# Performance work log

Measured on AMD Instinct MI355X. Metric: run time of the kernel, lower is better.

## Reference

```python
import jax, jax.numpy as jnp
import numpy as np

# Config (matches init_kwargs)
COV_DIM = 4
EMBED = 64
E = 256            # key_value_size / MHA embed dim
LH = 512           # lstm_hidden_dim
NH = 8             # num_heads
DH = E // NH
PS = 48            # predict_steps
START = 336        # predict_start
IN1 = 1 + COV_DIM + EMBED + E  # lstm1 input size = 325


def lstm_cell(x, h, c, w_ih, w_hh, b_ih, b_hh):
    gates = x @ w_ih.T + b_ih + h @ w_hh.T + b_hh
    i, f, g, o = jnp.split(gates, 4, axis=-1)
    c = jax.nn.sigmoid(f) * c + jax.nn.sigmoid(i) * jnp.tanh(g)
    h = jax.nn.sigmoid(o) * jnp.tanh(c)
    return h, c


def setup_inputs() -> dict:
    key = jax.random.key(0)
    ks = jax.random.split(key, 24)
    B, T = 512, 336
    s = 0.05
    return {
        "zxs": jax.random.normal(ks[0], (B, START + PS, 1 + COV_DIM), jnp.float32),
        "key": jax.random.normal(ks[1], (B, T, E), jnp.float32),
        "value": jax.random.normal(ks[2], (B, T, E), jnp.float32),
        "idx_embed": jax.random.normal(ks[3], (B, EMBED), jnp.float32),
        # lstm1: input IN1 -> hidden LH
        "w_ih1": jax.random.normal(ks[4], (4 * LH, IN1), jnp.float32) * s,
        "w_hh1": jax.random.normal(ks[5], (4 * LH, LH), jnp.float32) * s,
        "b_ih1": jax.random.normal(ks[6], (4 * LH,), jnp.float32) * s,
        "b_hh1": jax.random.normal(ks[7], (4 * LH,), jnp.float32) * s,
        # lstm2: input LH -> hidden E
        "w_ih2": jax.random.normal(ks[8], (4 * E, LH), jnp.float32) * s,
        "w_hh2": jax.random.normal(ks[9], (4 * E, E), jnp.float32) * s,
        "b_ih2": jax.random.normal(ks[10], (4 * E,), jnp.float32) * s,
        "b_hh2": jax.random.normal(ks[11], (4 * E,), jnp.float32) * s,
        # MultiheadAttention packed in-proj (q,k,v) + out proj
        "in_proj_w": jax.random.normal(ks[12], (3 * E, E), jnp.float32) * s,
        "in_proj_b": jax.random.normal(ks[13], (3 * E,), jnp.float32) * s,
        "out_proj_w": jax.random.normal(ks[14], (E, E), jnp.float32) * s,
        "out_proj_b": jax.random.normal(ks[15], (E,), jnp.float32) * s,
        # heads: Linear(2E -> 1)
        "mu_w": jax.random.normal(ks[16], (1, 2 * E), jnp.float32) * s,
        "mu_b": jax.random.normal(ks[17], (1,), jnp.float32) * s,
        "ps_w": jax.random.normal(ks[18], (1, 2 * E), jnp.float32) * s,
        "ps_b": jax.random.normal(ks[19], (1,), jnp.float32) * s,
    }


def reference(zxs, key, value, idx_embed,
              w_ih1, w_hh1, b_ih1, b_hh1,
              w_ih2, w_hh2, b_ih2, b_hh2,
              in_proj_w, in_proj_b, out_proj_w, out_proj_b,
              mu_w, mu_b, ps_w, ps_b):
    B, T, _ = key.shape
    dt = key.dtype
    wq, wk, wv = jnp.split(in_proj_w, 3, axis=0)
    bq, bk, bv = jnp.split(in_proj_b, 3)
    # K/V projections are constant across decode steps: hoist out of loop.
    kp = (key @ wk.T + bk).reshape(B, T, NH, DH).transpose(0, 2, 1, 3)   # (B,H,T,DH)
    vp = (value @ wv.T + bv).reshape(B, T, NH, DH).transpose(0, 2, 1, 3)  # (B,H,T,DH)
    xs = zxs[:, START:START + PS, :].transpose(1, 0, 2)  # (PS,B,1+cov)
    scale = 1.0 / np.sqrt(DH).astype(np.float32)

    carry0 = (jnp.zeros((B, LH), dt), jnp.zeros((B, LH), dt),
              jnp.zeros((B, E), dt), jnp.zeros((B, E), dt),
              jnp.zeros((B, E), dt))

    def step(carry, x):
        h1, c1, h2, c2, ctx = carry
        inp = jnp.concatenate([x, idx_embed, ctx], axis=1)
        h1, c1 = lstm_cell(inp, h1, c1, w_ih1, w_hh1, b_ih1, b_hh1)
        h2, c2 = lstm_cell(h1, h2, c2, w_ih2, w_hh2, b_ih2, b_hh2)
        # single-query multihead cross-attention (dropout=eval/identity)
        q = (h2 @ wq.T + bq).reshape(B, NH, DH)
        attn = jax.nn.softmax(jnp.einsum('bhd,bhtd->bht', q, kp) * scale, axis=-1)
        ctx = jnp.einsum('bht,bhtd->bhd', attn, vp).reshape(B, E) @ out_proj_w.T + out_proj_b
        oc = jnp.concatenate([h2, ctx], axis=1)  # (B, 2E)
        mu = oc @ mu_w.T + mu_b                  # (B,1)
        sigma = jax.nn.softplus(oc @ ps_w.T + ps_b)
        attn_avg = attn.mean(axis=1)             # head-averaged weights (B,T)
        return (h1, c1, h2, c2, ctx), (mu[:, 0], sigma[:, 0], attn_avg[0])

    _, (mus, sigmas, attns) = jax.lax.scan(step, carry0, xs)
    pred_mu = mus.T        # (B, PS)
    pred_sigma = sigmas.T  # (B, PS)
    attentions = attns.T   # (T, PS) -- matches torch.stack(list of (T,), dim=1)
    return pred_mu, pred_sigma, attentions
```

## Files before the change

### kernel.cpp

```cpp
#include <hip/hip_runtime.h>
#include <hip/hip_bf16.h>

#define BB    512
#define TTT   336
#define EE    256
#define LHH   512
#define NHH   8
#define DHH   32
#define PSS   48
#define STARTT 336
#define NCOV  5
#define XW1   352
#define KP1   864
#define KP2   768
#define COFF  69

typedef __hip_bfloat16 bf16;
typedef __bf16 bf16x8 __attribute__((ext_vector_type(8)));
typedef float  f32x4  __attribute__((ext_vector_type(4)));

__device__ __forceinline__ float sigf(float x) { return 1.f / (1.f + __expf(-x)); }
__device__ __forceinline__ float bf2lo(unsigned u) { return __uint_as_float(u << 16); }
__device__ __forceinline__ float bf2hi(unsigned u) { return __uint_as_float(u & 0xffff0000u); }

__global__ void k_zero(float* __restrict__ p, int n) {
    for (int i = blockIdx.x * blockDim.x + threadIdx.x; i < n; i += gridDim.x * blockDim.x)
        p[i] = 0.f;
}

__global__ void k_cvt_wc1(const float* __restrict__ wih, const float* __restrict__ whh,
                          bf16* __restrict__ Wc) {
    int i = blockIdx.x * blockDim.x + threadIdx.x;
    if (i >= 2048 * KP1) return;
    int n = i / KP1, k = i % KP1;
    float v = (k < 325) ? wih[n * 325 + k] : ((k >= 352) ? whh[n * 512 + (k - 352)] : 0.f);
    Wc[i] = __float2bfloat16(v);
}

__global__ void k_cvt_wc2(const float* __restrict__ wih, const float* __restrict__ whh,
                          bf16* __restrict__ Wc) {
    int i = blockIdx.x * blockDim.x + threadIdx.x;
    if (i >= 1024 * KP2) return;
    int n = i / KP2, k = i % KP2;
    float v = (k < 512) ? wih[n * 512 + k] : whh[n * 256 + (k - 512)];
    Wc[i] = __float2bfloat16(v);
}

__global__ void k_cvt(const float* __restrict__ src, bf16* __restrict__ dst, int n) {
    int i = blockIdx.x * blockDim.x + threadIdx.x;
    if (i < n) dst[i] = __float2bfloat16(src[i]);
}

__global__ void k_bsum(const float* __restrict__ a, const float* __restrict__ b,
                       float* __restrict__ o, int n) {
    int i = blockIdx.x * blockDim.x + threadIdx.x;
    if (i < n) o[i] = a[i] + b[i];
}

__global__ void k_init_xh1(bf16* __restrict__ xh1, const float* __restrict__ idx_embed,
                           const float* __restrict__ zxs) {
    int i = blockIdx.x * blockDim.x + threadIdx.x;
    if (i >= BB * XW1) return;
    int b = i / XW1, k = i % XW1;
    float v = 0.f;
    if (k < NCOV)      v = zxs[b * ((STARTT + PSS) * NCOV) + STARTT * NCOV + k];
    else if (k < COFF) v = idx_embed[b * 64 + (k - NCOV)];
    xh1[i] = __float2bfloat16(v);
}

template<int H, int K0T, int K1T>
__global__ __launch_bounds__(256)
void k_lstm_step(const bf16* __restrict__ A0, int ld0,
                 const bf16* __restrict__ A1, int ld1,
                 const bf16* __restrict__ Wc, const float* __restrict__ bsum,
                 float* __restrict__ c, bf16* __restrict__ hdst,
                 float* __restrict__ outF) {
    constexpr int KP = (K0T + K1T) * 32;
    __shared__ __align__(16) bf16 As[64 * 32];
    __shared__ __align__(16) bf16 Bs[256 * 32];
    const int tid = threadIdx.x;
    const int w = tid >> 6, l = tid & 63;
    const int row0 = blockIdx.x * 64, col0 = blockIdx.y * 64;
    const int srow = tid >> 2, schunk = tid & 3;
    const int fr = l & 15, fc = l >> 4;
    f32x4 acc[16] = {};

    for (int kt = 0; kt < K0T + K1T; ++kt) {
        {
            const bf16* base = (kt < K0T) ? A0 : A1;
            const int ldx    = (kt < K0T) ? ld0 : ld1;
            const int kk     = (kt < K0T) ? kt : (kt - K0T);
            uint4 va = *(const uint4*)(base + (size_t)(row0 + srow) * ldx + kk * 32 + schunk * 8);
            *(uint4*)(As + srow * 32 + (((schunk + (srow >> 1)) & 3) << 3)) = va;
        }
        #pragma unroll
        for (int i = 0; i < 4; ++i) {
            int n = i * 64 + srow;
            int gr = (n >> 6) * H + col0 + (n & 63);
            uint4 vb = *(const uint4*)(Wc + (size_t)gr * KP + kt * 32 + schunk * 8);
            *(uint4*)(Bs + n * 32 + (((schunk + (n >> 1)) & 3) << 3)) = vb;
        }
        __syncthreads();
        const int ar = w * 16 + fr;
        bf16x8 a = *(const bf16x8*)(As + ar * 32 + (((fc + (ar >> 1)) & 3) << 3));
        #pragma unroll
        for (int nt = 0; nt < 16; ++nt) {
            const int br = nt * 16 + fr;
            bf16x8 b = *(const bf16x8*)(Bs + br * 32 + (((fc + (br >> 1)) & 3) << 3));
            acc[nt] = __builtin_amdgcn_mfma_f32_16x16x32_bf16(a, b, acc[nt], 0, 0, 0);
        }
        __syncthreads();
    }

    #pragma unroll
    for (int u = 0; u < 4; ++u) {
        const int hu = col0 + u * 16 + fr;
        const float bi = bsum[hu], bff = bsum[H + hu], bg = bsum[2 * H + hu], bo = bsum[3 * H + hu];
        #pragma unroll
        for (int r = 0; r < 4; ++r) {
            const int R = row0 + w * 16 + fc * 4 + r;
            float gi = acc[u][r]      + bi;
            float gf = acc[4 + u][r]  + bff;
            float gg = acc[8 + u][r]  + bg;
            float go = acc[12 + u][r] + bo;
            float cn = sigf(gf) * c[(size_t)R * H + hu] + sigf(gi) * tanhf(gg);
            c[(size_t)R * H + hu] = cn;
            float h = sigf(go) * tanhf(cn);
            hdst[(size_t)R * H + hu] = __float2bfloat16(h);
            if (outF) outF[(size_t)R * H + hu] = h;
        }
    }
}

__global__ __launch_bounds__(256)
void k_kvproj(const float* __restrict__ X, const bf16* __restrict__ Wb,
              const float* __restrict__ bias, bf16* __restrict__ out) {
    __shared__ __align__(16) bf16 As[64 * 32];
    __shared__ __align__(16) bf16 Bs[256 * 32];
    const int tid = threadIdx.x;
    const int w = tid >> 6, l = tid & 63;
    const int row0 = blockIdx.x * 64;
    const int srow = tid >> 2, schunk = tid & 3;
    const int fr = l & 15, fc = l >> 4;
    f32x4 acc[16] = {};

    for (int kt = 0; kt < 8; ++kt) {
        {
            const float* ap = X + (size_t)(row0 + srow) * EE + kt * 32 + schunk * 8;
            float4 v0 = *(const float4*)ap, v1 = *(const float4*)(ap + 4);
            union { bf16 h[8]; uint4 u; } pk;
            pk.h[0] = __float2bfloat16(v0.x); pk.h[1] = __float2bfloat16(v0.y);
            pk.h[2] = __float2bfloat16(v0.z); pk.h[3] = __float2bfloat16(v0.w);
            pk.h[4] = __float2bfloat16(v1.x); pk.h[5] = __float2bfloat16(v1.y);
            pk.h[6] = __float2bfloat16(v1.z); pk.h[7] = __float2bfloat16(v1.w);
            *(uint4*)(As + srow * 32 + (((schunk + (srow >> 1)) & 3) << 3)) = pk.u;
        }
        #pragma unroll
        for (int i = 0; i < 4; ++i) {
            int n = i * 64 + srow;
            uint4 vb = *(const uint4*)(Wb + (size_t)n * EE + kt * 32 + schunk * 8);
            *(uint4*)(Bs + n * 32 + (((schunk + (n >> 1)) & 3) << 3)) = vb;
        }
        __syncthreads();
        const int ar = w * 16 + fr;
        bf16x8 a = *(const bf16x8*)(As + ar * 32 + (((fc + (ar >> 1)) & 3) << 3));
        #pragma unroll
        for (int nt = 0; nt < 16; ++nt) {
            const int br = nt * 16 + fr;
            bf16x8 b = *(const bf16x8*)(Bs + br * 32 + (((fc + (br >> 1)) & 3) << 3));
            acc[nt] = __builtin_amdgcn_mfma_f32_16x16x32_bf16(a, b, acc[nt], 0, 0, 0);
        }
        __syncthreads();
    }
    #pragma unroll
    for (int nt = 0; nt < 16; ++nt) {
        const int col = nt * 16 + fr;
        const float bv = bias[col];
        #pragma unroll
        for (int r = 0; r < 4; ++r) {
            const int R = row0 + w * 16 + fc * 4 + r;
            out[(size_t)R * EE + col] = __float2bfloat16(acc[nt][r] + bv);
        }
    }
}

__global__ __launch_bounds__(256)
void k_attn_out(const float* __restrict__ h2f, const float* __restrict__ wq, const float* __restrict__ bq,
                const bf16* __restrict__ kp, const bf16* __restrict__ vp,
                const float* __restrict__ opw, const float* __restrict__ opb,
                const float* __restrict__ mu_w, const float* __restrict__ mu_b,
                const float* __restrict__ ps_w, const float* __restrict__ ps_b,
                const float* __restrict__ zxs, bf16* __restrict__ xh1,
                float* __restrict__ out_mu, float* __restrict__ out_sigma,
                float* __restrict__ attn_out, int step) {
    const int b = blockIdx.x;
    const int tid = threadIdx.x;
    __shared__ float h2s[EE];
    __shared__ float qs[EE];
    __shared__ float s[NHH][TTT];
    __shared__ float rm[4], rp[4];

    h2s[tid] = h2f[(size_t)b * EE + tid];
    __syncthreads();

    {
        const float* wr = wq + (size_t)tid * EE;
        float acc = bq[tid];
        #pragma unroll 8
        for (int i = 0; i < EE; ++i) acc += h2s[i] * wr[i];
        qs[tid] = acc * 0.17677669529663689f;
    }
    __syncthreads();

    for (int p = tid; p < NHH * TTT; p += 256) {
        const int h = p / TTT, t = p % TTT;
        const uint4* kr = reinterpret_cast<const uint4*>(kp + ((size_t)(b * TTT + t)) * EE + h * DHH);
        const float* qh = qs + h * DHH;
        float acc = 0.f;
        #pragma unroll
        for (int r = 0; r < 4; ++r) {
            uint4 v = kr[r];
            acc += bf2lo(v.x) * qh[8 * r + 0] + bf2hi(v.x) * qh[8 * r + 1];
            acc += bf2lo(v.y) * qh[8 * r + 2] + bf2hi(v.y) * qh[8 * r + 3];
            acc += bf2lo(v.z) * qh[8 * r + 4] + bf2hi(v.z) * qh[8 * r + 5];
            acc += bf2lo(v.w) * qh[8 * r + 6] + bf2hi(v.w) * qh[8 * r + 7];
        }
        s[h][t] = acc;
    }
    __syncthreads();

    {
        const int wv = tid >> 6, lane = tid & 63;
        for (int hh = 0; hh < 2; ++hh) {
            const int h = wv * 2 + hh;
            float m = -1e30f;
            for (int t = lane; t < TTT; t += 64) m = fmaxf(m, s[h][t]);
            #pragma unroll
            for (int o = 32; o; o >>= 1) m = fmaxf(m, __shfl_xor(m, o));
            float sum = 0.f;
            for (int t = lane; t < TTT; t += 64) {
                float e = __expf(s[h][t] - m);
                s[h][t] = e;
                sum += e;
            }
            #pragma unroll
            for (int o = 32; o; o >>= 1) sum += __shfl_xor(sum, o);
            const float inv = 1.f / sum;
            for (int t = lane; t < TTT; t += 64) s[h][t] *= inv;
        }
    }
    __syncthreads();

    if (b == 0) {
        for (int t = tid; t < TTT; t += 256) {
            float a = 0.f;
            #pragma unroll
            for (int h = 0; h < NHH; ++h) a += s[h][t];
            attn_out[t * PSS + step] = a * 0.125f;
        }
    }

    float av;
    {
        const int h = tid >> 5, d = tid & 31;
        const bf16* vb = vp + (size_t)b * TTT * EE + h * DHH + d;
        float acc = 0.f;
        #pragma unroll 8
        for (int t = 0; t < TTT; ++t)
            acc += s[h][t] * __bfloat162float(vb[(size_t)t * EE]);
        av = acc;
    }
    qs[tid] = av;
    __syncthreads();

    {
        const float* wr = opw + (size_t)tid * EE;
        float ctxv = opb[tid];
        #pragma unroll 8
        for (int i = 0; i < EE; ++i) ctxv += qs[i] * wr[i];
        xh1[(size_t)b * XW1 + COFF + tid] = __float2bfloat16(ctxv);

        const float hv = h2s[tid];
        float pm = hv * mu_w[tid] + ctxv * mu_w[EE + tid];
        float pp = hv * ps_w[tid] + ctxv * ps_w[EE + tid];
        #pragma unroll
        for (int o = 32; o; o >>= 1) {
            pm += __shfl_xor(pm, o);
            pp += __shfl_xor(pp, o);
        }
        const int wv = tid >> 6, lane = tid & 63;
        if (lane == 0) { rm[wv] = pm; rp[wv] = pp; }
    }
    __syncthreads();
    if (tid == 0) {
        float m = rm[0] + rm[1] + rm[2] + rm[3] + mu_b[0];
        float p = rp[0] + rp[1] + rp[2] + rp[3] + ps_b[0];
        out_mu[b * PSS + step] = m;
        out_sigma[b * PSS + step] = (p > 20.f) ? p : log1pf(__expf(p));
    }

    if (tid < NCOV && step + 1 < PSS)
        xh1[(size_t)b * XW1 + tid] =
            __float2bfloat16(zxs[b * ((STARTT + PSS) * NCOV) + (STARTT + step + 1) * NCOV + tid]);
}

extern "C" void kernel_launch(void* const* d_in, const int* in_sizes, int n_in,
                              void* d_out, int out_size, void* d_ws, size_t ws_size,
                              hipStream_t stream) {
    const float* zxs       = (const float*)d_in[0];
    const float* key       = (const float*)d_in[1];
    const float* value     = (const float*)d_in[2];
    const float* idx_embed = (const float*)d_in[3];
    const float* w_ih1     = (const float*)d_in[4];
    const float* w_hh1     = (const float*)d_in[5];
    const float* b_ih1     = (const float*)d_in[6];
    const float* b_hh1     = (const float*)d_in[7];
    const float* w_ih2     = (const float*)d_in[8];
    const float* w_hh2     = (const float*)d_in[9];
    const float* b_ih2     = (const float*)d_in[10];
    const float* b_hh2     = (const float*)d_in[11];
    const float* in_proj_w = (const float*)d_in[12];
    const float* in_proj_b = (const float*)d_in[13];
    const float* opw       = (const float*)d_in[14];
    const float* opb       = (const float*)d_in[15];
    const float* mu_w      = (const float*)d_in[16];
    const float* mu_b      = (const float*)d_in[17];
    const float* ps_w      = (const float*)d_in[18];
    const float* ps_b      = (const float*)d_in[19];
    float* out = (float*)d_out;

    char* ws = (char*)d_ws;
    bf16* kp    = (bf16*)ws;                       ws += (size_t)BB * TTT * EE * 2;
    bf16* vp    = (bf16*)ws;                       ws += (size_t)BB * TTT * EE * 2;
    bf16* wkvb  = (bf16*)ws;                       ws += (size_t)2 * EE * EE * 2;
    bf16* Wc1   = (bf16*)ws;                       ws += (size_t)2048 * KP1 * 2;
    bf16* Wc2   = (bf16*)ws;                       ws += (size_t)1024 * KP2 * 2;
    bf16* xh1   = (bf16*)ws;                       ws += (size_t)BB * XW1 * 2;
    bf16* h1b0  = (bf16*)ws;                       ws += (size_t)BB * LHH * 2;
    bf16* h1b1  = (bf16*)ws;                       ws += (size_t)BB * LHH * 2;
    bf16* h2b0  = (bf16*)ws;                       ws += (size_t)BB * EE * 2;
    bf16* h2b1  = (bf16*)ws;                       ws += (size_t)BB * EE * 2;
    float* c1   = (float*)ws;                      ws += (size_t)BB * LHH * 4;
    float* c2   = (float*)ws;                      ws += (size_t)BB * EE * 4;
    float* h2f  = (float*)ws;                      ws += (size_t)BB * EE * 4;
    float* bsum1 = (float*)ws;                     ws += 4 * LHH * 4;
    float* bsum2 = (float*)ws;                     ws += 4 * EE * 4;
    bf16* h1buf[2] = { h1b0, h1b1 };
    bf16* h2buf[2] = { h2b0, h2b1 };

    const float* bq = in_proj_b;
    const float* bk = in_proj_b + EE;
    const float* bv = in_proj_b + 2 * EE;
    const float* wq = in_proj_w;

    k_cvt_wc1<<<(2048 * KP1 + 255) / 256, 256, 0, stream>>>(w_ih1, w_hh1, Wc1);
    k_cvt_wc2<<<(1024 * KP2 + 255) / 256, 256, 0, stream>>>(w_ih2, w_hh2, Wc2);
    k_cvt<<<(2 * EE * EE + 255) / 256, 256, 0, stream>>>(in_proj_w + EE * EE, wkvb, 2 * EE * EE);
    k_bsum<<<(4 * LHH + 255) / 256, 256, 0, stream>>>(b_ih1, b_hh1, bsum1, 4 * LHH);
    k_bsum<<<(4 * EE + 255) / 256, 256, 0, stream>>>(b_ih2, b_hh2, bsum2, 4 * EE);
    k_init_xh1<<<(BB * XW1 + 255) / 256, 256, 0, stream>>>(xh1, idx_embed, zxs);
    k_zero<<<1024, 256, 0, stream>>>((float*)h1b0, (2 * BB * LHH + 2 * BB * EE) / 2);
    k_zero<<<1024, 256, 0, stream>>>(c1, BB * LHH + BB * EE);

    k_kvproj<<<BB * TTT / 64, 256, 0, stream>>>(key, wkvb, bk, kp);
    k_kvproj<<<BB * TTT / 64, 256, 0, stream>>>(value, wkvb + EE * EE, bv, vp);

    for (int t = 0; t < PSS; ++t) {
        const int p = t & 1, q = (t + 1) & 1;
        k_lstm_step<LHH, XW1 / 32, LHH / 32><<<dim3(BB / 64, LHH / 64), 256, 0, stream>>>(
            xh1, XW1, h1buf[p], LHH, Wc1, bsum1, c1, h1buf[q], nullptr);
        k_lstm_step<EE, LHH / 32, EE / 32><<<dim3(BB / 64, EE / 64), 256, 0, stream>>>(
            h1buf[q], LHH, h2buf[p], EE, Wc2, bsum2, c2, h2buf[q], h2f);
        k_attn_out<<<BB, 256, 0, stream>>>(h2f, wq, bq, kp, vp, opw, opb,
                                           mu_w, mu_b, ps_w, ps_b, zxs, xh1,
                                           out, out + BB * PSS, out + 2 * BB * PSS, t);
    }
}
```

Baseline: 6.545 ms.

## Coalesce K/V reads in attention and use bf16 Q/out-proj weights

Restructures the per-batch attention kernel so each group of 32 threads reads one full contiguous K/V row with 16-byte loads. The score dot products are combined with warp shuffles, and the attention-times-V partials are reduced through shared memory. Q and output-projection weights are pre-converted to bf16 and read as vectorised uint4 loads, halving their traffic. This targets the strided, poorly coalesced K/V and weight reads in the per-step attention kernel, at the cost of lower weight precision and extra syncs.

Result: faster. 5.793 ms (-11.5%).

```diff
diff --git a/kernel.cpp b/kernel.cpp
--- a/kernel.cpp
+++ b/kernel.cpp
@@ -14,6 +14,7 @@
 #define KP1   864
 #define KP2   768
 #define COFF  69
+#define SPAD  340
 
 typedef __hip_bfloat16 bf16;
 typedef __bf16 bf16x8 __attribute__((ext_vector_type(8)));
@@ -185,9 +186,9 @@
 }
 
 __global__ __launch_bounds__(256)
-void k_attn_out(const float* __restrict__ h2f, const float* __restrict__ wq, const float* __restrict__ bq,
+void k_attn_out(const float* __restrict__ h2f, const bf16* __restrict__ wqb, const float* __restrict__ bq,
                 const bf16* __restrict__ kp, const bf16* __restrict__ vp,
-                const float* __restrict__ opw, const float* __restrict__ opb,
+                const bf16* __restrict__ opwb, const float* __restrict__ opb,
                 const float* __restrict__ mu_w, const float* __restrict__ mu_b,
                 const float* __restrict__ ps_w, const float* __restrict__ ps_b,
                 const float* __restrict__ zxs, bf16* __restrict__ xh1,
@@ -197,35 +198,43 @@
     const int tid = threadIdx.x;
     __shared__ float h2s[EE];
     __shared__ float qs[EE];
-    __shared__ float s[NHH][TTT];
+    __shared__ float s[NHH][SPAD];
     __shared__ float rm[4], rp[4];
 
     h2s[tid] = h2f[(size_t)b * EE + tid];
     __syncthreads();
 
     {
-        const float* wr = wq + (size_t)tid * EE;
+        const uint4* wr = (const uint4*)(wqb + (size_t)tid * EE);
         float acc = bq[tid];
-        #pragma unroll 8
-        for (int i = 0; i < EE; ++i) acc += h2s[i] * wr[i];
+        #pragma unroll
+        for (int i = 0; i < EE / 8; ++i) {
+            uint4 v = wr[i];
+            const float* hh = h2s + i * 8;
+            acc += bf2lo(v.x) * hh[0] + bf2hi(v.x) * hh[1] + bf2lo(v.y) * hh[2] + bf2hi(v.y) * hh[3]
+                 + bf2lo(v.z) * hh[4] + bf2hi(v.z) * hh[5] + bf2lo(v.w) * hh[6] + bf2hi(v.w) * hh[7];
+        }
         qs[tid] = acc * 0.17677669529663689f;
     }
     __syncthreads();
 
-    for (int p = tid; p < NHH * TTT; p += 256) {
-        const int h = p / TTT, t = p % TTT;
-        const uint4* kr = reinterpret_cast<const uint4*>(kp + ((size_t)(b * TTT + t)) * EE + h * DHH);
-        const float* qh = qs + h * DHH;
-        float acc = 0.f;
-        #pragma unroll
-        for (int r = 0; r < 4; ++r) {
-            uint4 v = kr[r];
-            acc += bf2lo(v.x) * qh[8 * r + 0] + bf2hi(v.x) * qh[8 * r + 1];
-            acc += bf2lo(v.y) * qh[8 * r + 2] + bf2hi(v.y) * qh[8 * r + 3];
-            acc += bf2lo(v.z) * qh[8 * r + 4] + bf2hi(v.z) * qh[8 * r + 5];
-            acc += bf2lo(v.w) * qh[8 * r + 6] + bf2hi(v.w) * qh[8 * r + 7];
-        }
-        s[h][t] = acc;
+    const int tt = tid >> 5, ck = tid & 31;
+    const int head = ck >> 2;
+
+    {
+        float q0 = qs[ck * 8 + 0], q1 = qs[ck * 8 + 1], q2 = qs[ck * 8 + 2], q3 = qs[ck * 8 + 3];
+        float q4 = qs[ck * 8 + 4], q5 = qs[ck * 8 + 5], q6 = qs[ck * 8 + 6], q7 = qs[ck * 8 + 7];
+        const bf16* kb = kp + (size_t)b * TTT * EE;
+        #pragma unroll 3
+        for (int t0 = 0; t0 < TTT; t0 += 8) {
+            const int t = t0 + tt;
+            uint4 v = *(const uint4*)(kb + (size_t)t * EE + ck * 8);
+            float p = bf2lo(v.x) * q0 + bf2hi(v.x) * q1 + bf2lo(v.y) * q2 + bf2hi(v.y) * q3
+                    + bf2lo(v.z) * q4 + bf2hi(v.z) * q5 + bf2lo(v.w) * q6 + bf2hi(v.w) * q7;
+            p += __shfl_xor(p, 1);
+            p += __shfl_xor(p, 2);
+            if ((ck & 3) == 0) s[head][t] = p;
+        }
     }
     __syncthreads();
 
@@ -260,24 +269,50 @@
         }
     }
 
-    float av;
-    {
-        const int h = tid >> 5, d = tid & 31;
-        const bf16* vb = vp + (size_t)b * TTT * EE + h * DHH + d;
-        float acc = 0.f;
-        #pragma unroll 8
-        for (int t = 0; t < TTT; ++t)
-            acc += s[h][t] * __bfloat162float(vb[(size_t)t * EE]);
-        av = acc;
-    }
-    qs[tid] = av;
-    __syncthreads();
-
-    {
-        const float* wr = opw + (size_t)tid * EE;
+    float a0 = 0.f, a1 = 0.f, a2 = 0.f, a3 = 0.f, a4 = 0.f, a5 = 0.f, a6 = 0.f, a7 = 0.f;
+    {
+        const bf16* vb = vp + (size_t)b * TTT * EE;
+        #pragma unroll 3
+        for (int t0 = 0; t0 < TTT; t0 += 8) {
+            const int t = t0 + tt;
+            uint4 v = *(const uint4*)(vb + (size_t)t * EE + ck * 8);
+            const float a = s[head][t];
+            a0 += a * bf2lo(v.x); a1 += a * bf2hi(v.x);
+            a2 += a * bf2lo(v.y); a3 += a * bf2hi(v.y);
+            a4 += a * bf2lo(v.z); a5 += a * bf2hi(v.z);
+            a6 += a * bf2lo(v.w); a7 += a * bf2hi(v.w);
+        }
+    }
+    __syncthreads();
+    {
+        float* red = &s[0][0];
+        red[0 * 256 + tt * 32 + ck] = a0;
+        red[1 * 256 + tt * 32 + ck] = a1;
+        red[2 * 256 + tt * 32 + ck] = a2;
+        red[3 * 256 + tt * 32 + ck] = a3;
+        red[4 * 256 + tt * 32 + ck] = a4;
+        red[5 * 256 + tt * 32 + ck] = a5;
+        red[6 * 256 + tt * 32 + ck] = a6;
+        red[7 * 256 + tt * 32 + ck] = a7;
+        __syncthreads();
+        float av = 0.f;
+        #pragma unroll
+        for (int k = 0; k < 8; ++k) av += red[tt * 256 + k * 32 + ck];
+        __syncthreads();
+        qs[ck * 8 + tt] = av;
+    }
+    __syncthreads();
+
+    {
+        const uint4* wr = (const uint4*)(opwb + (size_t)tid * EE);
         float ctxv = opb[tid];
-        #pragma unroll 8
-        for (int i = 0; i < EE; ++i) ctxv += qs[i] * wr[i];
+        #pragma unroll
+        for (int i = 0; i < EE / 8; ++i) {
+            uint4 v = wr[i];
+            const float* hh = qs + i * 8;
+            ctxv += bf2lo(v.x) * hh[0] + bf2hi(v.x) * hh[1] + bf2lo(v.y) * hh[2] + bf2hi(v.y) * hh[3]
+                  + bf2lo(v.z) * hh[4] + bf2hi(v.z) * hh[5] + bf2lo(v.w) * hh[6] + bf2hi(v.w) * hh[7];
+        }
         xh1[(size_t)b * XW1 + COFF + tid] = __float2bfloat16(ctxv);
 
         const float hv = h2s[tid];
@@ -333,6 +368,8 @@
     bf16* kp    = (bf16*)ws;                       ws += (size_t)BB * TTT * EE * 2;
     bf16* vp    = (bf16*)ws;                       ws += (size_t)BB * TTT * EE * 2;
     bf16* wkvb  = (bf16*)ws;                       ws += (size_t)2 * EE * EE * 2;
+    bf16* wqb   = (bf16*)ws;                       ws += (size_t)EE * EE * 2;
+    bf16* opwb  = (bf16*)ws;                       ws += (size_t)EE * EE * 2;
     bf16* Wc1   = (bf16*)ws;                       ws += (size_t)2048 * KP1 * 2;
     bf16* Wc2   = (bf16*)ws;                       ws += (size_t)1024 * KP2 * 2;
     bf16* xh1   = (bf16*)ws;                       ws += (size_t)BB * XW1 * 2;
@@ -351,11 +388,12 @@
     const float* bq = in_proj_b;
     const float* bk = in_proj_b + EE;
     const float* bv = in_proj_b + 2 * EE;
-    const float* wq = in_proj_w;
 
     k_cvt_wc1<<<(2048 * KP1 + 255) / 256, 256, 0, stream>>>(w_ih1, w_hh1, Wc1);
     k_cvt_wc2<<<(1024 * KP2 + 255) / 256, 256, 0, stream>>>(w_ih2, w_hh2, Wc2);
     k_cvt<<<(2 * EE * EE + 255) / 256, 256, 0, stream>>>(in_proj_w + EE * EE, wkvb, 2 * EE * EE);
+    k_cvt<<<(EE * EE + 255) / 256, 256, 0, stream>>>(in_proj_w, wqb, EE * EE);
+    k_cvt<<<(EE * EE + 255) / 256, 256, 0, stream>>>(opw, opwb, EE * EE);
     k_bsum<<<(4 * LHH + 255) / 256, 256, 0, stream>>>(b_ih1, b_hh1, bsum1, 4 * LHH);
     k_bsum<<<(4 * EE + 255) / 256, 256, 0, stream>>>(b_ih2, b_hh2, bsum2, 4 * EE);
     k_init_xh1<<<(BB * XW1 + 255) / 256, 256, 0, stream>>>(xh1, idx_embed, zxs);
@@ -371,7 +409,7 @@
             xh1, XW1, h1buf[p], LHH, Wc1, bsum1, c1, h1buf[q], nullptr);
         k_lstm_step<EE, LHH / 32, EE / 32><<<dim3(BB / 64, EE / 64), 256, 0, stream>>>(
             h1buf[q], LHH, h2buf[p], EE, Wc2, bsum2, c2, h2buf[q], h2f);
-        k_attn_out<<<BB, 256, 0, stream>>>(h2f, wq, bq, kp, vp, opw, opb,
+        k_attn_out<<<BB, 256, 0, stream>>>(h2f, wqb, bq, kp, vp, opwb, opb,
                                            mu_w, mu_b, ps_w, ps_b, zxs, xh1,
                                            out, out + BB * PSS, out + 2 * BB * PSS, t);
     }
```
